# Performance work log

Measured on AMD Instinct MI355X. Metric: run time of the kernel, lower is better.

The kernel has to match this reference:

```python
import jax, jax.numpy as jnp
import numpy as np

N = 10000        # nodes
E = 160000       # active edges
NS = 128         # scalar (0e) channels per tensor
NV = 64          # vector (1o) channels per tensor
LAT = 64         # latent dim
AVG_NEIGH = 16.0
SQ2 = float(np.sqrt(2.0))
SQ3 = float(np.sqrt(3.0))
EPS = 1e-5


def setup_inputs() -> dict:
    key = jax.random.key(0)
    ks = jax.random.split(key, 24)
    rn = lambda k, s: jax.random.normal(k, s, jnp.float32)
    d = {}
    d["latents"] = rn(ks[0], (E, LAT))
    d["node_features"] = rn(ks[1], (N, NS + 3 * NV))
    d["edge_features"] = rn(ks[2], (E, NS + 3 * NV))
    d["edge_sh"] = rn(ks[3], (E, 4))
    d["edge_index"] = jax.random.randint(ks[4], (2, E), 0, N)
    d["atom_type"] = jax.random.randint(ks[5], (N,), 0, 10)
    d["active_edges"] = jnp.arange(E)
    # separable layer norm affine params (node and edge)
    d["g_s_n"] = jnp.ones((NS,), jnp.float32); d["b_s_n"] = jnp.zeros((NS,), jnp.float32)
    d["g_v_n"] = jnp.ones((NV,), jnp.float32)
    d["g_s_e"] = jnp.ones((NS,), jnp.float32); d["b_s_e"] = jnp.zeros((NS,), jnp.float32)
    d["g_v_e"] = jnp.ones((NV,), jnp.float32)
    # FullyConnectedTensorProduct weights (path-normalized init).
    # tp input: 2*NS scalars, 2*NV vectors; sh: 1 scalar + 1 vector;
    # tp output: NS+NV scalars (scalars+gates), NV vectors.
    nSt, nVt, nSo = 2 * NS, 2 * NV, NS + NV
    d["W_ss0"] = rn(ks[6], (nSt, nSo)) / np.sqrt(nSt * 2)
    d["W_vv0"] = rn(ks[7], (nVt, nSo)) / np.sqrt(nVt * 2)
    d["W_sv1"] = rn(ks[8], (nSt, NV)) / np.sqrt(nSt * 3)
    d["W_vs1"] = rn(ks[9], (nVt, NV)) / np.sqrt(nVt * 3)
    d["W_vv1"] = rn(ks[10], (nVt, NV)) / np.sqrt(nVt * 3)
    # lin_post (per-l channel mixing)
    d["Wp_s"] = rn(ks[11], (NS, NS)) / np.sqrt(NS)
    d["Wp_v"] = rn(ks[12], (NV, NV)) / np.sqrt(NV)
    # env_embed_mlps: single linear latent -> weight_numel (NS+NV channels)
    d["W_env"] = rn(ks[13], (LAT, NS + NV)) / np.sqrt(LAT)
    # linear_res
    d["Wr_s"] = rn(ks[14], (NS, NS)) / np.sqrt(NS)
    d["Wr_v"] = rn(ks[15], (NV, NV)) / np.sqrt(NV)
    return d


def _sep_ln(x, g_s, b_s, g_v):
    # separable layer norm: standard LN on scalars, RMS-of-norms on vectors
    s = x[:, :NS]
    v = x[:, NS:].reshape(-1, NV, 3)
    mu = s.mean(-1, keepdims=True)
    var = ((s - mu) ** 2).mean(-1, keepdims=True)
    s = (s - mu) * jax.lax.rsqrt(var + EPS) * g_s + b_s
    vn = jnp.mean(jnp.sum(v * v, -1), -1, keepdims=True)  # (B,1)
    v = v * jax.lax.rsqrt(vn + EPS)[:, :, None] * g_v[None, :, None]
    return s, v


def _forward(latents, node_features, edge_features, edge_sh, edge_index,
             atom_type, active_edges,
             g_s_n, b_s_n, g_v_n, g_s_e, b_s_e, g_v_e,
             W_ss0, W_vv0, W_sv1, W_vs1, W_vv1,
             Wp_s, Wp_v, W_env, Wr_s, Wr_v):
    ec = edge_index[0][active_edges]                      # (E,) center nodes
    ns, nv = _sep_ln(node_features, g_s_n, b_s_n, g_v_n)
    es, ev = _sep_ln(edge_features, g_s_e, b_s_e, g_v_e)
    S = jnp.concatenate([ns[ec], es], axis=-1)            # (E, 2*NS)
    V = jnp.concatenate([nv[ec], ev], axis=1)             # (E, 2*NV, 3)
    sh0 = edge_sh[:, :1]                                  # (E,1)
    sh1 = edge_sh[:, 1:]                                  # (E,3)
    # fully-connected tensor product (tp_in x sh -> gate input)
    dotV = jnp.einsum('ecd,ed->ec', V, sh1) / SQ3         # 1x1->0
    out0 = (S * sh0) @ W_ss0 + dotV @ W_vv0               # (E, NS+NV) scalars
    out_v = (S @ W_sv1)[:, :, None] * sh1[:, None, :]     # 0x1->1
    out_v = out_v + jnp.einsum('ecd,cf->efd', V, W_vs1) * sh0[:, :, None]  # 1x0->1
    cross = jnp.cross(V, sh1[:, None, :]) / SQ2           # 1x1->1
    out_v = out_v + jnp.einsum('ecd,cf->efd', cross, W_vv1)  # (E, NV, 3)
    # gate
    s = jax.nn.silu(out0[:, :NS])
    gates = jax.nn.sigmoid(out0[:, NS:])
    v = out_v * gates[:, :, None]
    # lin_post
    s = s @ Wp_s
    v = jnp.einsum('ecd,cf->efd', v, Wp_v)
    # env weights from latents (elementwise linear per channel)
    w = latents[active_edges] @ W_env                     # (E, NS+NV)
    s = s * w[:, :NS]
    v = v * w[:, NS:][:, :, None]
    msg = jnp.concatenate([s, v.reshape(-1, 3 * NV)], axis=-1)  # (E, 320)
    agg = jax.ops.segment_sum(msg, ec, num_segments=N)
    agg = agg * jnp.float32(1.0 / np.sqrt(AVG_NEIGH))
    # residual linear on raw node features
    rs = node_features[:, :NS] @ Wr_s
    rv = jnp.einsum('ncd,cf->nfd', node_features[:, NS:].reshape(-1, NV, 3), Wr_v)
    res = jnp.concatenate([rs, rv.reshape(-1, 3 * NV)], axis=-1)
    return res + agg


def reference(latents, node_features, edge_features, edge_sh, edge_index,
              atom_type, active_edges,
              g_s_n, b_s_n, g_v_n, g_s_e, b_s_e, g_v_e,
              W_ss0, W_vv0, W_sv1, W_vs1, W_vv1,
              Wp_s, Wp_v, W_env, Wr_s, Wr_v):
    return _forward(latents, node_features, edge_features, edge_sh, edge_index,
                    atom_type, active_edges,
                    g_s_n, b_s_n, g_v_n, g_s_e, b_s_e, g_v_e,
                    W_ss0, W_vv0, W_sv1, W_vs1, W_vv1,
                    Wp_s, Wp_v, W_env, Wr_s, Wr_v)
```

## Files before the change

kernel.cpp:

```cpp
#include <hip/hip_runtime.h>

#define N_NODES 10000
#define N_EDGES 160000
#define NSC 128
#define ROW 320
#define EPS_LN 1e-5f
#define INV_SQ2 0.70710678118654752440f
#define INV_SQ3 0.57735026918962576451f

typedef unsigned short bfraw;
typedef __attribute__((ext_vector_type(8))) short short8;
typedef __attribute__((ext_vector_type(4))) float float4x;
typedef __attribute__((ext_vector_type(2))) float float2x;

__device__ __forceinline__ float bf2f(bfraw u) {
    union { unsigned int i; float f; } x; x.i = ((unsigned int)u) << 16; return x.f;
}
__device__ __forceinline__ bfraw f2bf(float f) {
    union { float f; unsigned int i; } x; x.f = f;
    unsigned int i = x.i;
    unsigned int lsb = (i >> 16) & 1u;
    i += 0x7fffu + lsb;
    return (bfraw)(i >> 16);
}
template<bool B> __device__ __forceinline__ float LD(const void* p, size_t i) {
    if (B) return bf2f(((const bfraw*)p)[i]);
    else   return ((const float*)p)[i];
}
template<bool B> __device__ __forceinline__ void ST(void* p, size_t i, float v) {
    if (B) ((bfraw*)p)[i] = f2bf(v);
    else   ((float*)p)[i] = v;
}
__device__ __forceinline__ float wred64(float v) {
#pragma unroll
    for (int o = 32; o > 0; o >>= 1) v += __shfl_xor(v, o, 64);
    return v;
}
__device__ __forceinline__ void wredx12(float a[12]) {
#pragma unroll
    for (int o = 32; o > 0; o >>= 1) {
        float t[12];
#pragma unroll
        for (int i = 0; i < 12; i++) t[i] = __shfl_xor(a[i], o, 64);
#pragma unroll
        for (int i = 0; i < 12; i++) a[i] += t[i];
    }
}
__device__ __forceinline__ float silu_f(float x) { return x / (1.0f + __expf(-x)); }
__device__ __forceinline__ float sigm_f(float x) { return 1.0f / (1.0f + __expf(-x)); }

#define MFMA16(a, b, c) __builtin_amdgcn_mfma_f32_16x16x32_bf16((a), (b), (c), 0, 0, 0)

__device__ __forceinline__ int SDI(int r, int c) { return r * 384 + (c ^ ((r & 7) << 3)); }
__device__ __forceinline__ int X64(int r, int c) { return r * 64  + (c ^ ((r & 7) << 3)); }
__device__ __forceinline__ int SPI(int r, int c) { return r * 128 + (c ^ ((r & 7) << 3)); }
__device__ __forceinline__ int WVI(int r, int c) { return r * 192 + (c ^ ((r & 7) << 2)); }

__device__ __forceinline__ int dtype_flag(const void* g_s_n) {
    return (((const unsigned int*)g_s_n)[0] == 0x3F803F80u) ? 1 : 0;
}

__device__ __forceinline__ void pack_body(int idx, int fl,
    const void* Wss0, const void* Wvv0, const void* Wsv1, const void* Wvs1,
    const void* Wvv1, const void* Wps,  const void* Wpv,  const void* Wenv,
    const void* Wrs,  const void* Wrv,  bfraw* __restrict__ dst)
{
    const void* src; int K, N, base;
    if      (idx <  49152) { src = Wss0; K = 256; N = 192; base = 0; }
    else if (idx <  73728) { src = Wvv0; K = 128; N = 192; base = 49152; }
    else if (idx <  90112) { src = Wsv1; K = 256; N =  64; base = 73728; }
    else if (idx <  98304) { src = Wvs1; K = 128; N =  64; base = 90112; }
    else if (idx < 106496) { src = Wvv1; K = 128; N =  64; base = 98304; }
    else if (idx < 122880) { src = Wps;  K = 128; N = 128; base = 106496; }
    else if (idx < 126976) { src = Wpv;  K =  64; N =  64; base = 122880; }
    else if (idx < 139264) { src = Wenv; K =  64; N = 192; base = 126976; }
    else if (idx < 155648) { src = Wrs;  K = 128; N = 128; base = 139264; }
    else                   { src = Wrv;  K =  64; N =  64; base = 155648; }
    int li = idx - base;
    int j = li & 7, l = (li >> 3) & 63, t = li >> 9;
    int NT = N >> 4;
    int nt = t % NT, kt = t / NT;
    int k = kt * 32 + ((l >> 4) << 3) + j;
    int n = (nt << 4) + (l & 15);
    float v = fl ? bf2f(((const bfraw*)src)[(size_t)k * N + n])
                 : ((const float*)src)[(size_t)k * N + n];
    dst[idx] = f2bf(v);
}

template<bool B>
__device__ __forceinline__ void node_ln_body(int n, int lane,
    const void* nf, const void* g_s, const void* b_s, const void* g_v,
    float* __restrict__ nsnv)
{
    size_t base = (size_t)n * ROW;
    float s0 = LD<B>(nf, base + lane), s1 = LD<B>(nf, base + 64 + lane);
    float mu = wred64(s0 + s1) * (1.0f / 128.0f);
    float d0 = s0 - mu, d1 = s1 - mu;
    float var = wred64(d0 * d0 + d1 * d1) * (1.0f / 128.0f);
    float rs = rsqrtf(var + EPS_LN);
    float o0 = d0 * rs * LD<B>(g_s, lane) + LD<B>(b_s, lane);
    float o1 = d1 * rs * LD<B>(g_s, 64 + lane) + LD<B>(b_s, 64 + lane);
    float vx = LD<B>(nf, base + NSC + 3 * lane);
    float vy = LD<B>(nf, base + NSC + 3 * lane + 1);
    float vz = LD<B>(nf, base + NSC + 3 * lane + 2);
    float vn = wred64(vx * vx + vy * vy + vz * vz) * (1.0f / 64.0f);
    float rv = rsqrtf(vn + EPS_LN) * LD<B>(g_v, lane);
    float* o = nsnv + base;
    o[lane] = o0; o[64 + lane] = o1;
    o[NSC + 3 * lane] = vx * rv; o[NSC + 3 * lane + 1] = vy * rv; o[NSC + 3 * lane + 2] = vz * rv;
}

__global__ __launch_bounds__(256) void prep_k(
    const void* Wss0, const void* Wvv0, const void* Wsv1, const void* Wvs1,
    const void* Wvv1, const void* Wps,  const void* Wpv,  const void* Wenv,
    const void* Wrs,  const void* Wrv,  bfraw* __restrict__ pk,
    const int* __restrict__ eidx, const int* __restrict__ act, int* __restrict__ counts,
    const void* nf, const void* g_s_n, const void* b_s_n, const void* g_v_n,
    float* __restrict__ nsnv)
{
    int fl = dtype_flag(g_s_n);
    int idx = blockIdx.x * 256 + threadIdx.x;
    if (idx < 159744)
        pack_body(idx, fl, Wss0, Wvv0, Wsv1, Wvs1, Wvv1, Wps, Wpv, Wenv, Wrs, Wrv, pk);
    if (idx < N_EDGES)
        atomicAdd(&counts[eidx[act[idx]]], 1);
    int w = threadIdx.x >> 6, lane = threadIdx.x & 63;
    int n = blockIdx.x * 4 + w;
    if (fl) node_ln_body<true >(n, lane, nf, g_s_n, b_s_n, g_v_n, nsnv);
    else    node_ln_body<false>(n, lane, nf, g_s_n, b_s_n, g_v_n, nsnv);
}

__global__ __launch_bounds__(1024) void scan_k(const int* __restrict__ counts,
                                               int* __restrict__ starts) {
    __shared__ int wsum[16];
    int t = threadIdx.x;
    int lo = t * 10;
    int lanev = t & 63, wv = t >> 6;
    int c[10];
    int s = 0;
    if (lo < N_NODES) {
#pragma unroll
        for (int j = 0; j < 10; j++) { c[j] = counts[lo + j]; s += c[j]; }
    }
    int ps = s;
#pragma unroll
    for (int o = 1; o < 64; o <<= 1) {
        int u = __shfl_up(ps, o, 64);
        if (lanev >= o) ps += u;
    }
    if (lanev == 63) wsum[wv] = ps;
    __syncthreads();
    if (t == 0) {
        int acc = 0;
#pragma unroll
        for (int i = 0; i < 16; i++) { int v = wsum[i]; wsum[i] = acc; acc += v; }
        starts[N_NODES] = acc;
    }
    __syncthreads();
    if (lo < N_NODES) {
        int acc = wsum[wv] + ps - s;
#pragma unroll
        for (int j = 0; j < 10; j++) { starts[lo + j] = acc; acc += c[j]; }
    }
}

__global__ void fill_k(const int* __restrict__ eidx, const int* __restrict__ act,
                       const int* __restrict__ starts, int* __restrict__ cursor,
                       int* __restrict__ csr) {
    int e = blockIdx.x * 256 + threadIdx.x;
    if (e < N_EDGES) {
        int n = eidx[act[e]];
        int pos = atomicAdd(&cursor[n], 1);
        csr[starts[n] + pos] = e;
    }
}

template<bool B>
__device__ void edge_body(char* smem, int tid,
    const float* __restrict__ nsnv,
    const void* ef, const void* esh,
    const int* __restrict__ eidx, const int* __restrict__ act,
    const void* lat,
    const void* g_s_e, const void* b_s_e, const void* g_v_e,
    const bfraw* __restrict__ pk,
    bfraw* __restrict__ msg)
{
    bfraw* SD     = (bfraw*)(smem);
    bfraw* Vn     = (bfraw*)(smem + 12288);
    bfraw* Ve     = (bfraw*)(smem + 18432);
    bfraw* gate_u = (bfraw*)(smem + 18432);
    bfraw* sp_u   = (bfraw*)(smem + 20480);
    bfraw* lat_u  = (bfraw*)(smem + 24576);
    float* sh_f   = (float*)(smem + 26624);
    float* wenv_f = (float*)(smem);

    const bfraw* pWss0 = pk;
    const bfraw* pWvv0 = pk + 49152;
    const bfraw* pWsv1 = pk + 73728;
    const bfraw* pWvs1 = pk + 90112;
    const bfraw* pWvv1 = pk + 98304;
    const bfraw* pWps  = pk + 106496;
    const bfraw* pWpv  = pk + 122880;
    const bfraw* pWenv = pk + 126976;

    const int w = tid >> 6, lane = tid & 63;
    const int nl = lane & 15, mq = lane >> 4;
    const int e0 = blockIdx.x * 16;

    float gse0 = LD<B>(g_s_e, lane), gse1 = LD<B>(g_s_e, 64 + lane);
    float bse0 = LD<B>(b_s_e, lane), bse1 = LD<B>(b_s_e, 64 + lane);
    float gve  = LD<B>(g_v_e, lane);

    int ae_[4], cn_[4];
#pragma unroll
    for (int i = 0; i < 4; i++) ae_[i] = act[e0 + w * 4 + i];
#pragma unroll
    for (int i = 0; i < 4; i++) cn_[i] = eidx[ae_[i]];

    float es0[4], es1[4], ex[4], ey[4], ez[4];
    float shv[4][4];
#pragma unroll
    for (int i = 0; i < 4; i++) {
        int el = w * 4 + i, e = e0 + el;
        shv[i][0] = LD<B>(esh, (size_t)e * 4 + 0);
        shv[i][1] = LD<B>(esh, (size_t)e * 4 + 1);
        shv[i][2] = LD<B>(esh, (size_t)e * 4 + 2);
        shv[i][3] = LD<B>(esh, (size_t)e * 4 + 3);
        size_t eb = (size_t)e * ROW;
        es0[i] = LD<B>(ef, eb + lane);
        es1[i] = LD<B>(ef, eb + 64 + lane);
        ex[i]  = LD<B>(ef, eb + NSC + 3 * lane);
        ey[i]  = LD<B>(ef, eb + NSC + 3 * lane + 1);
        ez[i]  = LD<B>(ef, eb + NSC + 3 * lane + 2);
        float la = LD<B>(lat, (size_t)ae_[i] * 64 + lane);
        const float* nr = nsnv + (size_t)cn_[i] * ROW;
        float n0 = nr[lane], n1 = nr[64 + lane];
        float nx = nr[NSC + 3 * lane], ny = nr[NSC + 3 * lane + 1], nz = nr[NSC + 3 * lane + 2];
        SD[SDI(el, lane)]       = f2bf(n0);
        SD[SDI(el, 64 + lane)]  = f2bf(n1);
        SD[SDI(el, 256 + lane)] = f2bf((nx * shv[i][1] + ny * shv[i][2] + nz * shv[i][3]) * INV_SQ3);
        Vn[X64(el, lane)]       = f2bf(nx);
        Vn[X64(16 + el, lane)]  = f2bf(ny);
        Vn[X64(32 + el, lane)]  = f2bf(nz);
        lat_u[X64(el, lane)]    = f2bf(la);
        if (lane == 0) {
            sh_f[el * 4]     = shv[i][0]; sh_f[el * 4 + 1] = shv[i][1];
            sh_f[el * 4 + 2] = shv[i][2]; sh_f[el * 4 + 3] = shv[i][3];
        }
    }
    float red[12];
#pragma unroll
    for (int i = 0; i < 4; i++) {
        red[i]     = es0[i] + es1[i];
        red[4 + i] = es0[i] * es0[i] + es1[i] * es1[i];
        red[8 + i] = ex[i] * ex[i] + ey[i] * ey[i] + ez[i] * ez[i];
    }
    wredx12(red);
#pragma unroll
    for (int i = 0; i < 4; i++) {
        int el = w * 4 + i;
        float mu  = red[i] * (1.0f / 128.0f);
        float var = red[4 + i] * (1.0f / 128.0f) - mu * mu;
        float rs  = rsqrtf(var + EPS_LN);
        float o0  = (es0[i] - mu) * rs * gse0 + bse0;
        float o1  = (es1[i] - mu) * rs * gse1 + bse1;
        float rv  = rsqrtf(red[8 + i] * (1.0f / 64.0f) + EPS_LN) * gve;
        float exn = ex[i] * rv, eyn = ey[i] * rv, ezn = ez[i] * rv;
        SD[SDI(el, 128 + lane)] = f2bf(o0);
        SD[SDI(el, 192 + lane)] = f2bf(o1);
        SD[SDI(el, 320 + lane)] = f2bf((exn * shv[i][1] + eyn * shv[i][2] + ezn * shv[i][3]) * INV_SQ3);
        Ve[X64(el, lane)]       = f2bf(exn);
        Ve[X64(16 + el, lane)]  = f2bf(eyn);
        Ve[X64(32 + el, lane)]  = f2bf(ezn);
    }
    __syncthreads();

    float4x sA0={0,0,0,0}, sA1={0,0,0,0}, sA2={0,0,0,0}, cSV={0,0,0,0};
    {
        const bfraw* ps = pWss0 + (size_t)(3 * w * 64 + lane) * 8;
        const bfraw* pv = pWsv1 + (size_t)(w * 64 + lane) * 8;
        short8 b0[4], b1[4];
#define LDG1(kt, D) do { \
        D[0] = *(const short8*)(ps + (kt) * 6144);        \
        D[1] = *(const short8*)(ps + (kt) * 6144 + 512);  \
        D[2] = *(const short8*)(ps + (kt) * 6144 + 1024); \
        D[3] = *(const short8*)(pv + (kt) * 2048); } while (0)
        LDG1(0, b0); LDG1(1, b1);
#pragma unroll
        for (int kt = 0; kt < 8; kt++) {
            short8 a = *(const short8*)&SD[SDI(nl, kt * 32 + mq * 8)];
            if ((kt & 1) == 0) {
                sA0 = MFMA16(a, b0[0], sA0); sA1 = MFMA16(a, b0[1], sA1);
                sA2 = MFMA16(a, b0[2], sA2); cSV = MFMA16(a, b0[3], cSV);
                if (kt + 2 < 8) LDG1(kt + 2, b0);
            } else {
                sA0 = MFMA16(a, b1[0], sA0); sA1 = MFMA16(a, b1[1], sA1);
                sA2 = MFMA16(a, b1[2], sA2); cSV = MFMA16(a, b1[3], cSV);
                if (kt + 2 < 8) LDG1(kt + 2, b1);
            }
        }
#undef LDG1
    }
    float4x dA0={0,0,0,0}, dA1={0,0,0,0}, dA2={0,0,0,0};
    {
        const bfraw* pd = pWvv0 + (size_t)(3 * w * 64 + lane) * 8;
        short8 c0[3], c1[3];
#define LDGD(kt, D) do { \
        D[0] = *(const short8*)(pd + (kt) * 6144);        \
        D[1] = *(const short8*)(pd + (kt) * 6144 + 512);  \
        D[2] = *(const short8*)(pd + (kt) * 6144 + 1024); } while (0)
        LDGD(0, c0); LDGD(1, c1);
#pragma unroll
        for (int kt = 0; kt < 4; kt++) {
            short8 a = *(const short8*)&SD[SDI(nl, 256 + kt * 32 + mq * 8)];
            if ((kt & 1) == 0) {
                dA0 = MFMA16(a, c0[0], dA0); dA1 = MFMA16(a, c0[1], dA1); dA2 = MFMA16(a, c0[2], dA2);
                if (kt + 2 < 4) LDGD(kt + 2, c0);
            } else {
                dA0 = MFMA16(a, c1[0], dA0); dA1 = MFMA16(a, c1[1], dA1); dA2 = MFMA16(a, c1[2], dA2);
                if (kt + 2 < 4) LDGD(kt + 2, c1);
            }
        }
#undef LDGD
    }
    float o_g1[3][4];
#pragma unroll
    for (int r = 0; r < 4; r++) {
        float sh0 = sh_f[(mq * 4 + r) * 4];
        o_g1[0][r] = sh0 * sA0[r] + dA0[r];
        o_g1[1][r] = sh0 * sA1[r] + dA1[r];
        o_g1[2][r] = sh0 * sA2[r] + dA2[r];
    }
    float4x H[3] = {{0,0,0,0},{0,0,0,0},{0,0,0,0}};
    float4x K[3] = {{0,0,0,0},{0,0,0,0},{0,0,0,0}};
    {
        const bfraw* ph = pWvs1 + (size_t)(w * 64 + lane) * 8;
        const bfraw* pq = pWvv1 + (size_t)(w * 64 + lane) * 8;
        short8 gH0 = *(const short8*)(ph);
        short8 gH1 = *(const short8*)(ph + 2048);
        short8 gH2 = *(const short8*)(ph + 4096);
        short8 gH3 = *(const short8*)(ph + 6144);
        short8 gK0 = *(const short8*)(pq);
        short8 gK1 = *(const short8*)(pq + 2048);
        short8 gK2 = *(const short8*)(pq + 4096);
        short8 gK3 = *(const short8*)(pq + 6144);
#pragma unroll
        for (int d = 0; d < 3; d++) {
            short8 a0 = *(const short8*)&Vn[X64(d * 16 + nl, mq * 8)];
            short8 a1 = *(const short8*)&Vn[X64(d * 16 + nl, 32 + mq * 8)];
            short8 a2 = *(const short8*)&Ve[X64(d * 16 + nl, mq * 8)];
            short8 a3 = *(const short8*)&Ve[X64(d * 16 + nl, 32 + mq * 8)];
            H[d] = MFMA16(a0, gH0, H[d]); K[d] = MFMA16(a0, gK0, K[d]);
            H[d] = MFMA16(a1, gH1, H[d]); K[d] = MFMA16(a1, gK1, K[d]);
            H[d] = MFMA16(a2, gH2, H[d]); K[d] = MFMA16(a2, gK2, K[d]);
            H[d] = MFMA16(a3, gH3, H[d]); K[d] = MFMA16(a3, gK3, K[d]);
        }
    }
    __syncthreads();

#pragma unroll
    for (int t = 0; t < 3; t++) {
        int tile = 3 * w + t;
#pragma unroll
        for (int r = 0; r < 4; r++) {
            int el = mq * 4 + r;
            float o = o_g1[t][r];
            if (tile < 8) sp_u[SPI(el, tile * 16 + nl)]         = f2bf(silu_f(o));
            else          gate_u[X64(el, (tile - 8) * 16 + nl)] = f2bf(sigm_f(o));
        }
    }
    __syncthreads();

    {
        int f = w * 16 + nl;
#pragma unroll
        for (int r = 0; r < 4; r++) {
            int el = mq * 4 + r;
            float g   = bf2f(gate_u[X64(el, f)]);
            float svv = cSV[r];
            float s0v = sh_f[el * 4], b0 = sh_f[el * 4 + 1], b1 = sh_f[el * 4 + 2], b2 = sh_f[el * 4 + 3];
            float ov0 = svv * b0 + s0v * H[0][r] + (b2 * K[1][r] - b1 * K[2][r]) * INV_SQ2;
            float ov1 = svv * b1 + s0v * H[1][r] + (b0 * K[2][r] - b2 * K[0][r]) * INV_SQ2;
            float ov2 = svv * b2 + s0v * H[2][r] + (b1 * K[0][r] - b0 * K[1][r]) * INV_SQ2;
            Vn[X64(el, f)]      = f2bf(ov0 * g);
            Vn[X64(16 + el, f)] = f2bf(ov1 * g);
            Vn[X64(32 + el, f)] = f2bf(ov2 * g);
        }
    }
    __syncthreads();

    float4x s2_0 = {0,0,0,0}, s2_1 = {0,0,0,0};
    {
        const bfraw* pp = pWps + (size_t)(w * 64 + lane) * 8;
        short8 u0[2], u1[2];
#define LDS2(kt, D) do { \
        D[0] = *(const short8*)(pp + (kt) * 4096);         \
        D[1] = *(const short8*)(pp + (kt) * 4096 + 2048); } while (0)
        LDS2(0, u0); LDS2(1, u1);
#pragma unroll
        for (int kt = 0; kt < 4; kt++) {
            short8 a = *(const short8*)&sp_u[SPI(nl, kt * 32 + mq * 8)];
            if ((kt & 1) == 0) {
                s2_0 = MFMA16(a, u0[0], s2_0); s2_1 = MFMA16(a, u0[1], s2_1);
                if (kt + 2 < 4) LDS2(kt + 2, u0);
            } else {
                s2_0 = MFMA16(a, u1[0], s2_0); s2_1 = MFMA16(a, u1[1], s2_1);
                if (kt + 2 < 4) LDS2(kt + 2, u1);
            }
        }
#undef LDS2
    }
    float4x wv0 = {0,0,0,0}, wv1 = {0,0,0,0}, wv2 = {0,0,0,0};
    {
        const bfraw* pe = pWenv + (size_t)(3 * w * 64 + lane) * 8;
        short8 e00 = *(const short8*)(pe);
        short8 e01 = *(const short8*)(pe + 512);
        short8 e02 = *(const short8*)(pe + 1024);
        short8 e10 = *(const short8*)(pe + 6144);
        short8 e11 = *(const short8*)(pe + 6144 + 512);
        short8 e12 = *(const short8*)(pe + 6144 + 1024);
        short8 a0 = *(const short8*)&lat_u[X64(nl, mq * 8)];
        short8 a1 = *(const short8*)&lat_u[X64(nl, 32 + mq * 8)];
        wv0 = MFMA16(a0, e00, wv0); wv0 = MFMA16(a1, e10, wv0);
        wv1 = MFMA16(a0, e01, wv1); wv1 = MFMA16(a1, e11, wv1);
        wv2 = MFMA16(a0, e02, wv2); wv2 = MFMA16(a1, e12, wv2);
    }
    float4x v2[3] = {{0,0,0,0},{0,0,0,0},{0,0,0,0}};
    {
        const bfraw* pz = pWpv + (size_t)(w * 64 + lane) * 8;
        short8 z0 = *(const short8*)(pz);
        short8 z1 = *(const short8*)(pz + 2048);
#pragma unroll
        for (int d = 0; d < 3; d++) {
            short8 a0 = *(const short8*)&Vn[X64(d * 16 + nl, mq * 8)];
            short8 a1 = *(const short8*)&Vn[X64(d * 16 + nl, 32 + mq * 8)];
            v2[d] = MFMA16(a0, z0, v2[d]);
            v2[d] = MFMA16(a1, z1, v2[d]);
        }
    }
    {
        float4x wvv[3] = {wv0, wv1, wv2};
#pragma unroll
        for (int t = 0; t < 3; t++)
#pragma unroll
            for (int r = 0; r < 4; r++)
                wenv_f[WVI(mq * 4 + r, (3 * w + t) * 16 + nl)] = wvv[t][r];
    }
    __syncthreads();

#pragma unroll
    for (int t = 0; t < 2; t++) {
        int c = (w + 4 * t) * 16 + nl;
        float4x s2v = (t == 0) ? s2_0 : s2_1;
#pragma unroll
        for (int r = 0; r < 4; r++) {
            int el = mq * 4 + r;
            msg[(size_t)(e0 + el) * 320 + c] = f2bf(s2v[r] * wenv_f[WVI(el, c)]);
        }
    }
    {
        int f = w * 16 + nl;
#pragma unroll
        for (int r = 0; r < 4; r++) {
            int el = mq * 4 + r;
            float we = wenv_f[WVI(el, 128 + f)];
            size_t base = (size_t)(e0 + el) * 320 + NSC + 3 * f;
            msg[base]     = f2bf(v2[0][r] * we);
            msg[base + 1] = f2bf(v2[1][r] * we);
            msg[base + 2] = f2bf(v2[2][r] * we);
        }
    }
}

__global__ __launch_bounds__(256, 4) void edge_mfma_k(
    const float* __restrict__ nsnv,
    const void* ef, const void* esh,
    const int* __restrict__ eidx, const int* __restrict__ act,
    const void* lat,
    const void* g_s_e, const void* b_s_e, const void* g_v_e,
    const bfraw* __restrict__ pk,
    bfraw* __restrict__ msg, const void* g_s_n)
{
    __shared__ __align__(16) char smem[26880];
    if (dtype_flag(g_s_n))
        edge_body<true >(smem, threadIdx.x, nsnv, ef, esh, eidx, act, lat,
                         g_s_e, b_s_e, g_v_e, pk, msg);
    else
        edge_body<false>(smem, threadIdx.x, nsnv, ef, esh, eidx, act, lat,
                         g_s_e, b_s_e, g_v_e, pk, msg);
}

__device__ __forceinline__ float lo16(unsigned u) { return bf2f((bfraw)(u & 0xffffu)); }
__device__ __forceinline__ float hi16(unsigned u) { return bf2f((bfraw)(u >> 16)); }

__global__ __launch_bounds__(256) void gather_k(
    const bfraw* __restrict__ msg, const int* __restrict__ starts,
    const int* __restrict__ csr, float* __restrict__ agg)
{
    int w = threadIdx.x >> 6, lane = threadIdx.x & 63;
    int n = blockIdx.x * 4 + w;
    if (n >= N_NODES) return;
    int s0 = starts[n], s1 = starts[n + 1];
    bool half = lane < 32;
    float l0 = 0, h0 = 0, l1 = 0, h1 = 0, l2 = 0, h2 = 0;
    int i = s0;
    for (; i + 1 < s1; i += 2) {
        const unsigned* r0 = (const unsigned*)(msg + (size_t)csr[i] * 320);
        const unsigned* r1 = (const unsigned*)(msg + (size_t)csr[i + 1] * 320);
        unsigned a00 = r0[lane], a01 = r0[64 + lane];
        unsigned a10 = r1[lane], a11 = r1[64 + lane];
        unsigned a02 = half ? r0[128 + lane] : 0u;
        unsigned a12 = half ? r1[128 + lane] : 0u;
        l0 += lo16(a00) + lo16(a10); h0 += hi16(a00) + hi16(a10);
        l1 += lo16(a01) + lo16(a11); h1 += hi16(a01) + hi16(a11);
        l2 += lo16(a02) + lo16(a12); h2 += hi16(a02) + hi16(a12);
    }
    if (i < s1) {
        const unsigned* r = (const unsigned*)(msg + (size_t)csr[i] * 320);
        unsigned a0 = r[lane], a1 = r[64 + lane];
        unsigned a2 = half ? r[128 + lane] : 0u;
        l0 += lo16(a0); h0 += hi16(a0);
        l1 += lo16(a1); h1 += hi16(a1);
        l2 += lo16(a2); h2 += hi16(a2);
    }
    float* o = agg + (size_t)n * ROW;
    float2x v0 = {l0, h0}, v1 = {l1, h1}, v2 = {l2, h2};
    ((float2x*)o)[lane] = v0;
    ((float2x*)(o + 128))[lane] = v1;
    if (half) ((float2x*)(o + 256))[lane] = v2;
}

template<bool B>
__device__ void final_body(char* smem, int tid,
    const void* nf, const float* __restrict__ agg,
    const bfraw* __restrict__ pk, void* out)
{
    bfraw* Sn_u = (bfraw*)(smem);
    bfraw* Vn_u = (bfraw*)(smem + 8704);
    const bfraw* pWrs = pk + 139264;
    const bfraw* pWrv = pk + 155648;

    const int w = tid >> 6, lane = tid & 63;
    const int nl = lane & 15, mq = lane >> 4;
    const int n0b = blockIdx.x * 32;

    for (int i = 0; i < 8; i++) {
        int el = w * 8 + i;
        int n = n0b + el;
        bool ok = n < N_NODES;
        size_t base = (size_t)n * ROW;
        float a0 = ok ? LD<B>(nf, base + lane) : 0.0f;
        float a1 = ok ? LD<B>(nf, base + 64 + lane) : 0.0f;
        float vx = ok ? LD<B>(nf, base + NSC + 3 * lane) : 0.0f;
        float vy = ok ? LD<B>(nf, base + NSC + 3 * lane + 1) : 0.0f;
        float vz = ok ? LD<B>(nf, base + NSC + 3 * lane + 2) : 0.0f;
        Sn_u[el * 136 + lane]      = f2bf(a0);
        Sn_u[el * 136 + 64 + lane] = f2bf(a1);
        Vn_u[(el) * 72 + lane]      = f2bf(vx);
        Vn_u[(32 + el) * 72 + lane] = f2bf(vy);
        Vn_u[(64 + el) * 72 + lane] = f2bf(vz);
    }
    __syncthreads();

    {
        const int mt = w & 1, ntb = (w >> 1) * 4;
        float4x c[4] = {{0,0,0,0},{0,0,0,0},{0,0,0,0},{0,0,0,0}};
#pragma unroll
        for (int kt = 0; kt < 4; kt++) {
            short8 a = *(const short8*)&Sn_u[(mt * 16 + nl) * 136 + kt * 32 + mq * 8];
#pragma unroll
            for (int t = 0; t < 4; t++) {
                short8 b = *(const short8*)&pWrs[((kt * 8 + ntb + t) * 64 + lane) * 8];
                c[t] = MFMA16(a, b, c[t]);
            }
        }
#pragma unroll
        for (int t = 0; t < 4; t++) {
            int cc = (ntb + t) * 16 + nl;
#pragma unroll
            for (int r = 0; r < 4; r++) {
                int n = n0b + mt * 16 + mq * 4 + r;
                if (n < N_NODES) {
                    size_t o = (size_t)n * ROW + cc;
                    ST<B>(out, o, c[t][r] + 0.25f * agg[o]);
                }
            }
        }
    }
    {
        float4x c[3][2] = {{{0,0,0,0},{0,0,0,0}},{{0,0,0,0},{0,0,0,0}},{{0,0,0,0},{0,0,0,0}}};
#pragma unroll
        for (int d = 0; d < 3; d++)
#pragma unroll
            for (int h = 0; h < 2; h++)
#pragma unroll
                for (int kt = 0; kt < 2; kt++) {
                    short8 a = *(const short8*)&Vn_u[(d * 32 + h * 16 + nl) * 72 + kt * 32 + mq * 8];
                    short8 b = *(const short8*)&pWrv[((kt * 4 + w) * 64 + lane) * 8];
                    c[d][h] = MFMA16(a, b, c[d][h]);
                }
        int f = w * 16 + nl;
#pragma unroll
        for (int h = 0; h < 2; h++)
#pragma unroll
            for (int r = 0; r < 4; r++) {
                int n = n0b + h * 16 + mq * 4 + r;
                if (n < N_NODES) {
                    size_t o = (size_t)n * ROW + NSC + 3 * f;
                    ST<B>(out, o,     c[0][h][r] + 0.25f * agg[o]);
                    ST<B>(out, o + 1, c[1][h][r] + 0.25f * agg[o + 1]);
                    ST<B>(out, o + 2, c[2][h][r] + 0.25f * agg[o + 2]);
                }
            }
    }
}

__global__ __launch_bounds__(256) void final_mfma_k(
    const void* nf, const float* __restrict__ agg,
    const bfraw* __restrict__ pk, void* out, const void* g_s_n)
{
    __shared__ __align__(16) char smem[22528];
    if (dtype_flag(g_s_n)) final_body<true >(smem, threadIdx.x, nf, agg, pk, out);
    else                   final_body<false>(smem, threadIdx.x, nf, agg, pk, out);
}

extern "C" void kernel_launch(void* const* d_in, const int* in_sizes, int n_in,
                              void* d_out, int out_size, void* d_ws, size_t ws_size,
                              hipStream_t stream)
{
    const void* latents = d_in[0];
    const void* node_f  = d_in[1];
    const void* edge_f  = d_in[2];
    const void* edge_sh = d_in[3];
    const int* edge_index = (const int*)d_in[4];
    const int* active     = (const int*)d_in[6];
    const void* g_s_n = d_in[7];
    const void* b_s_n = d_in[8];
    const void* g_v_n = d_in[9];
    const void* g_s_e = d_in[10];
    const void* b_s_e = d_in[11];
    const void* g_v_e = d_in[12];

    char* ws = (char*)d_ws;
    float* agg    = (float*)(ws + 256);
    float* nsnv   = (float*)(ws + 12800256);
    bfraw* pk     = (bfraw*)(ws + 25600256);
    int*   counts = (int*)(ws + 25919744);
    int*   cursor = (int*)(ws + 25960704);
    int*   starts = (int*)(ws + 26001664);
    int*   csr    = (int*)(ws + 26042624);
    bfraw* msg    = (bfraw*)(ws + 26682624);

    hipMemsetAsync(counts, 0, 81920, stream);
    prep_k<<<2500, 256, 0, stream>>>(d_in[13], d_in[14], d_in[15], d_in[16],
        d_in[17], d_in[18], d_in[19], d_in[20], d_in[21], d_in[22], pk,
        edge_index, active, counts, node_f, g_s_n, b_s_n, g_v_n, nsnv);
    scan_k<<<1, 1024, 0, stream>>>(counts, starts);
    fill_k<<<625, 256, 0, stream>>>(edge_index, active, starts, cursor, csr);
    edge_mfma_k<<<N_EDGES / 16, 256, 0, stream>>>(nsnv, edge_f, edge_sh, edge_index, active,
        latents, g_s_e, b_s_e, g_v_e, pk, msg, g_s_n);
    gather_k<<<N_NODES / 4, 256, 0, stream>>>(msg, starts, csr, agg);
    final_mfma_k<<<(N_NODES + 31) / 32, 256, 0, stream>>>(node_f, agg, pk, (void*)d_out, g_s_n);
}
```

Measured before the change: 581.4 us.

## Write edge messages in CSR order, store node LN in bf16, vectorize loads

fill_k now records each edge's destination slot in CSR order, and the edge kernel writes its message row directly to that slot. gather_k can then stream contiguous message rows per node instead of indirecting through a CSR index array. The normalized node features are stored as bf16 with paired scalars and planar vector components, which halves that buffer and lets the edge kernel copy node values into shared memory without conversion. Loads of features, spherical harmonics and latents are widened to 2/4-element vectors, node LN variance is computed from the mean of squares, and edge-kernel launch bounds rise to 6 blocks per CU, at the cost of scattered message writes and some extra register pressure.

```diff
diff --git a/kernel.cpp b/kernel.cpp
--- a/kernel.cpp
+++ b/kernel.cpp
@@ -23,6 +23,11 @@
     i += 0x7fffu + lsb;
     return (bfraw)(i >> 16);
 }
+__device__ __forceinline__ unsigned cvt_pk_bf16(float lo, float hi) {
+    unsigned r;
+    asm("v_cvt_pk_bf16_f32 %0, %1, %2" : "=v"(r) : "v"(lo), "v"(hi));
+    return r;
+}
 template<bool B> __device__ __forceinline__ float LD(const void* p, size_t i) {
     if (B) return bf2f(((const bfraw*)p)[i]);
     else   return ((const float*)p)[i];
@@ -30,6 +35,29 @@
 template<bool B> __device__ __forceinline__ void ST(void* p, size_t i, float v) {
     if (B) ((bfraw*)p)[i] = f2bf(v);
     else   ((float*)p)[i] = v;
+}
+template<bool B> __device__ __forceinline__ float2x LD2(const void* p, size_t i) {
+    float2x r;
+    if (B) {
+        unsigned u = *(const unsigned*)((const bfraw*)p + i);
+        r.x = bf2f((bfraw)(u & 0xffffu)); r.y = bf2f((bfraw)(u >> 16));
+    } else {
+        r = *(const float2x*)((const float*)p + i);
+    }
+    return r;
+}
+template<bool B> __device__ __forceinline__ float4x LD4(const void* p, size_t i) {
+    float4x r;
+    if (B) {
+        unsigned long long u = *(const unsigned long long*)((const bfraw*)p + i);
+        r.x = bf2f((bfraw)(u & 0xffffu));
+        r.y = bf2f((bfraw)((u >> 16) & 0xffffu));
+        r.z = bf2f((bfraw)((u >> 32) & 0xffffu));
+        r.w = bf2f((bfraw)(u >> 48));
+    } else {
+        r = *(const float4x*)((const float*)p + i);
+    }
+    return r;
 }
 __device__ __forceinline__ float wred64(float v) {
 #pragma unroll
@@ -90,24 +118,26 @@
 template<bool B>
 __device__ __forceinline__ void node_ln_body(int n, int lane,
     const void* nf, const void* g_s, const void* b_s, const void* g_v,
-    float* __restrict__ nsnv)
+    bfraw* __restrict__ nsnv)
 {
     size_t base = (size_t)n * ROW;
-    float s0 = LD<B>(nf, base + lane), s1 = LD<B>(nf, base + 64 + lane);
-    float mu = wred64(s0 + s1) * (1.0f / 128.0f);
-    float d0 = s0 - mu, d1 = s1 - mu;
-    float var = wred64(d0 * d0 + d1 * d1) * (1.0f / 128.0f);
-    float rs = rsqrtf(var + EPS_LN);
-    float o0 = d0 * rs * LD<B>(g_s, lane) + LD<B>(b_s, lane);
-    float o1 = d1 * rs * LD<B>(g_s, 64 + lane) + LD<B>(b_s, 64 + lane);
+    float2x s = LD2<B>(nf, base + 2 * lane);
+    float mu = wred64(s.x + s.y) * (1.0f / 128.0f);
+    float m2 = wred64(s.x * s.x + s.y * s.y) * (1.0f / 128.0f);
+    float rs = rsqrtf(m2 - mu * mu + EPS_LN);
+    float2x g = LD2<B>(g_s, 2 * lane), b = LD2<B>(b_s, 2 * lane);
+    float o0 = (s.x - mu) * rs * g.x + b.x;
+    float o1 = (s.y - mu) * rs * g.y + b.y;
     float vx = LD<B>(nf, base + NSC + 3 * lane);
     float vy = LD<B>(nf, base + NSC + 3 * lane + 1);
     float vz = LD<B>(nf, base + NSC + 3 * lane + 2);
     float vn = wred64(vx * vx + vy * vy + vz * vz) * (1.0f / 64.0f);
     float rv = rsqrtf(vn + EPS_LN) * LD<B>(g_v, lane);
-    float* o = nsnv + base;
-    o[lane] = o0; o[64 + lane] = o1;
-    o[NSC + 3 * lane] = vx * rv; o[NSC + 3 * lane + 1] = vy * rv; o[NSC + 3 * lane + 2] = vz * rv;
+    bfraw* row = nsnv + (size_t)n * 320;
+    ((unsigned*)row)[lane] = cvt_pk_bf16(o0, o1);
+    row[128 + lane] = f2bf(vx * rv);
+    row[192 + lane] = f2bf(vy * rv);
+    row[256 + lane] = f2bf(vz * rv);
 }
 
 __global__ __launch_bounds__(256) void prep_k(
@@ -116,7 +146,7 @@
     const void* Wrs,  const void* Wrv,  bfraw* __restrict__ pk,
     const int* __restrict__ eidx, const int* __restrict__ act, int* __restrict__ counts,
     const void* nf, const void* g_s_n, const void* b_s_n, const void* g_v_n,
-    float* __restrict__ nsnv)
+    bfraw* __restrict__ nsnv)
 {
     int fl = dtype_flag(g_s_n);
     int idx = blockIdx.x * 256 + threadIdx.x;
@@ -166,20 +196,21 @@
 
 __global__ void fill_k(const int* __restrict__ eidx, const int* __restrict__ act,
                        const int* __restrict__ starts, int* __restrict__ cursor,
-                       int* __restrict__ csr) {
+                       int* __restrict__ inv) {
     int e = blockIdx.x * 256 + threadIdx.x;
     if (e < N_EDGES) {
         int n = eidx[act[e]];
         int pos = atomicAdd(&cursor[n], 1);
-        csr[starts[n] + pos] = e;
+        inv[e] = starts[n] + pos;
     }
 }
 
 template<bool B>
 __device__ void edge_body(char* smem, int tid,
-    const float* __restrict__ nsnv,
+    const bfraw* __restrict__ nsnv,
     const void* ef, const void* esh,
     const int* __restrict__ eidx, const int* __restrict__ act,
+    const int* __restrict__ inv,
     const void* lat,
     const void* g_s_e, const void* b_s_e, const void* g_v_e,
     const bfraw* __restrict__ pk,
@@ -192,6 +223,7 @@
     bfraw* sp_u   = (bfraw*)(smem + 20480);
     bfraw* lat_u  = (bfraw*)(smem + 24576);
     float* sh_f   = (float*)(smem + 26624);
+    int*   slot_s = (int*)(smem + 26880);
     float* wenv_f = (float*)(smem);
 
     const bfraw* pWss0 = pk;
@@ -207,13 +239,12 @@
     const int nl = lane & 15, mq = lane >> 4;
     const int e0 = blockIdx.x * 16;
 
-    float gse0 = LD<B>(g_s_e, lane), gse1 = LD<B>(g_s_e, 64 + lane);
-    float bse0 = LD<B>(b_s_e, lane), bse1 = LD<B>(b_s_e, 64 + lane);
+    float2x gse = LD2<B>(g_s_e, 2 * lane), bse = LD2<B>(b_s_e, 2 * lane);
     float gve  = LD<B>(g_v_e, lane);
 
-    int ae_[4], cn_[4];
-#pragma unroll
-    for (int i = 0; i < 4; i++) ae_[i] = act[e0 + w * 4 + i];
+    int ae_[4], cn_[4], sl_[4];
+#pragma unroll
+    for (int i = 0; i < 4; i++) { ae_[i] = act[e0 + w * 4 + i]; sl_[i] = inv[e0 + w * 4 + i]; }
 #pragma unroll
     for (int i = 0; i < 4; i++) cn_[i] = eidx[ae_[i]];
 
@@ -222,30 +253,31 @@
 #pragma unroll
     for (int i = 0; i < 4; i++) {
         int el = w * 4 + i, e = e0 + el;
-        shv[i][0] = LD<B>(esh, (size_t)e * 4 + 0);
-        shv[i][1] = LD<B>(esh, (size_t)e * 4 + 1);
-        shv[i][2] = LD<B>(esh, (size_t)e * 4 + 2);
-        shv[i][3] = LD<B>(esh, (size_t)e * 4 + 3);
+        float4x sh = LD4<B>(esh, (size_t)e * 4);
+        shv[i][0] = sh.x; shv[i][1] = sh.y; shv[i][2] = sh.z; shv[i][3] = sh.w;
         size_t eb = (size_t)e * ROW;
-        es0[i] = LD<B>(ef, eb + lane);
-        es1[i] = LD<B>(ef, eb + 64 + lane);
+        float2x es = LD2<B>(ef, eb + 2 * lane);
+        es0[i] = es.x; es1[i] = es.y;
         ex[i]  = LD<B>(ef, eb + NSC + 3 * lane);
         ey[i]  = LD<B>(ef, eb + NSC + 3 * lane + 1);
         ez[i]  = LD<B>(ef, eb + NSC + 3 * lane + 2);
-        float la = LD<B>(lat, (size_t)ae_[i] * 64 + lane);
-        const float* nr = nsnv + (size_t)cn_[i] * ROW;
-        float n0 = nr[lane], n1 = nr[64 + lane];
-        float nx = nr[NSC + 3 * lane], ny = nr[NSC + 3 * lane + 1], nz = nr[NSC + 3 * lane + 2];
-        SD[SDI(el, lane)]       = f2bf(n0);
-        SD[SDI(el, 64 + lane)]  = f2bf(n1);
-        SD[SDI(el, 256 + lane)] = f2bf((nx * shv[i][1] + ny * shv[i][2] + nz * shv[i][3]) * INV_SQ3);
-        Vn[X64(el, lane)]       = f2bf(nx);
-        Vn[X64(16 + el, lane)]  = f2bf(ny);
-        Vn[X64(32 + el, lane)]  = f2bf(nz);
-        lat_u[X64(el, lane)]    = f2bf(la);
+        const bfraw* nr = nsnv + (size_t)cn_[i] * 320;
+        unsigned nsp = ((const unsigned*)nr)[lane];
+        bfraw nvx = nr[128 + lane], nvy = nr[192 + lane], nvz = nr[256 + lane];
+        float nx = bf2f(nvx), ny = bf2f(nvy), nz = bf2f(nvz);
+        *(unsigned*)&SD[SDI(el, 2 * lane)] = nsp;
+        SD[SDI(el, 256 + lane)] = f2bf((nx * sh.y + ny * sh.z + nz * sh.w) * INV_SQ3);
+        Vn[X64(el, lane)]      = nvx;
+        Vn[X64(16 + el, lane)] = nvy;
+        Vn[X64(32 + el, lane)] = nvz;
+        if (lane < 32) {
+            float2x la = LD2<B>(lat, (size_t)ae_[i] * 64 + 2 * lane);
+            *(unsigned*)&lat_u[X64(el, 2 * lane)] = cvt_pk_bf16(la.x, la.y);
+        }
         if (lane == 0) {
-            sh_f[el * 4]     = shv[i][0]; sh_f[el * 4 + 1] = shv[i][1];
-            sh_f[el * 4 + 2] = shv[i][2]; sh_f[el * 4 + 3] = shv[i][3];
+            sh_f[el * 4]     = sh.x; sh_f[el * 4 + 1] = sh.y;
+            sh_f[el * 4 + 2] = sh.z; sh_f[el * 4 + 3] = sh.w;
+            slot_s[el] = sl_[i];
         }
     }
     float red[12];
@@ -262,12 +294,11 @@
         float mu  = red[i] * (1.0f / 128.0f);
         float var = red[4 + i] * (1.0f / 128.0f) - mu * mu;
         float rs  = rsqrtf(var + EPS_LN);
-        float o0  = (es0[i] - mu) * rs * gse0 + bse0;
-        float o1  = (es1[i] - mu) * rs * gse1 + bse1;
+        float o0  = (es0[i] - mu) * rs * gse.x + bse.x;
+        float o1  = (es1[i] - mu) * rs * gse.y + bse.y;
         float rv  = rsqrtf(red[8 + i] * (1.0f / 64.0f) + EPS_LN) * gve;
         float exn = ex[i] * rv, eyn = ey[i] * rv, ezn = ez[i] * rv;
-        SD[SDI(el, 128 + lane)] = f2bf(o0);
-        SD[SDI(el, 192 + lane)] = f2bf(o1);
+        *(unsigned*)&SD[SDI(el, 128 + 2 * lane)] = cvt_pk_bf16(o0, o1);
         SD[SDI(el, 320 + lane)] = f2bf((exn * shv[i][1] + eyn * shv[i][2] + ezn * shv[i][3]) * INV_SQ3);
         Ve[X64(el, lane)]       = f2bf(exn);
         Ve[X64(16 + el, lane)]  = f2bf(eyn);
@@ -448,6 +479,9 @@
     }
     __syncthreads();
 
+    int mslot[4];
+#pragma unroll
+    for (int r = 0; r < 4; r++) mslot[r] = slot_s[mq * 4 + r];
 #pragma unroll
     for (int t = 0; t < 2; t++) {
         int c = (w + 4 * t) * 16 + nl;
@@ -455,7 +489,7 @@
 #pragma unroll
         for (int r = 0; r < 4; r++) {
             int el = mq * 4 + r;
-            msg[(size_t)(e0 + el) * 320 + c] = f2bf(s2v[r] * wenv_f[WVI(el, c)]);
+            msg[(size_t)mslot[r] * 320 + c] = f2bf(s2v[r] * wenv_f[WVI(el, c)]);
         }
     }
     {
@@ -464,7 +498,7 @@
         for (int r = 0; r < 4; r++) {
             int el = mq * 4 + r;
             float we = wenv_f[WVI(el, 128 + f)];
-            size_t base = (size_t)(e0 + el) * 320 + NSC + 3 * f;
+            size_t base = (size_t)mslot[r] * 320 + NSC + 3 * f;
             msg[base]     = f2bf(v2[0][r] * we);
             msg[base + 1] = f2bf(v2[1][r] * we);
             msg[base + 2] = f2bf(v2[2][r] * we);
@@ -472,21 +506,22 @@
     }
 }
 
-__global__ __launch_bounds__(256, 4) void edge_mfma_k(
-    const float* __restrict__ nsnv,
+__global__ __launch_bounds__(256, 6) void edge_mfma_k(
+    const bfraw* __restrict__ nsnv,
     const void* ef, const void* esh,
     const int* __restrict__ eidx, const int* __restrict__ act,
+    const int* __restrict__ inv,
     const void* lat,
     const void* g_s_e, const void* b_s_e, const void* g_v_e,
     const bfraw* __restrict__ pk,
     bfraw* __restrict__ msg, const void* g_s_n)
 {
-    __shared__ __align__(16) char smem[26880];
+    __shared__ __align__(16) char smem[26944];
     if (dtype_flag(g_s_n))
-        edge_body<true >(smem, threadIdx.x, nsnv, ef, esh, eidx, act, lat,
+        edge_body<true >(smem, threadIdx.x, nsnv, ef, esh, eidx, act, inv, lat,
                          g_s_e, b_s_e, g_v_e, pk, msg);
     else
-        edge_body<false>(smem, threadIdx.x, nsnv, ef, esh, eidx, act, lat,
+        edge_body<false>(smem, threadIdx.x, nsnv, ef, esh, eidx, act, inv, lat,
                          g_s_e, b_s_e, g_v_e, pk, msg);
 }
 
@@ -495,7 +530,7 @@
 
 __global__ __launch_bounds__(256) void gather_k(
     const bfraw* __restrict__ msg, const int* __restrict__ starts,
-    const int* __restrict__ csr, float* __restrict__ agg)
+    float* __restrict__ agg)
 {
     int w = threadIdx.x >> 6, lane = threadIdx.x & 63;
     int n = blockIdx.x * 4 + w;
@@ -503,25 +538,36 @@
     int s0 = starts[n], s1 = starts[n + 1];
     bool half = lane < 32;
     float l0 = 0, h0 = 0, l1 = 0, h1 = 0, l2 = 0, h2 = 0;
-    int i = s0;
-    for (; i + 1 < s1; i += 2) {
-        const unsigned* r0 = (const unsigned*)(msg + (size_t)csr[i] * 320);
-        const unsigned* r1 = (const unsigned*)(msg + (size_t)csr[i + 1] * 320);
-        unsigned a00 = r0[lane], a01 = r0[64 + lane];
-        unsigned a10 = r1[lane], a11 = r1[64 + lane];
-        unsigned a02 = half ? r0[128 + lane] : 0u;
-        unsigned a12 = half ? r1[128 + lane] : 0u;
-        l0 += lo16(a00) + lo16(a10); h0 += hi16(a00) + hi16(a10);
-        l1 += lo16(a01) + lo16(a11); h1 += hi16(a01) + hi16(a11);
-        l2 += lo16(a02) + lo16(a12); h2 += hi16(a02) + hi16(a12);
-    }
-    if (i < s1) {
-        const unsigned* r = (const unsigned*)(msg + (size_t)csr[i] * 320);
-        unsigned a0 = r[lane], a1 = r[64 + lane];
-        unsigned a2 = half ? r[128 + lane] : 0u;
-        l0 += lo16(a0); h0 += hi16(a0);
-        l1 += lo16(a1); h1 += hi16(a1);
-        l2 += lo16(a2); h2 += hi16(a2);
+    const unsigned* p = (const unsigned*)msg + (size_t)s0 * 160;
+    int cnt = s1 - s0;
+    int i = 0;
+    for (; i + 3 < cnt; i += 4) {
+        const unsigned* r0 = p + (size_t)i * 160;
+        const unsigned* r1 = r0 + 160;
+        const unsigned* r2 = r0 + 320;
+        const unsigned* r3 = r0 + 480;
+        unsigned a0 = r0[lane], b0 = r0[64 + lane];
+        unsigned a1 = r1[lane], b1 = r1[64 + lane];
+        unsigned a2 = r2[lane], b2 = r2[64 + lane];
+        unsigned a3 = r3[lane], b3 = r3[64 + lane];
+        unsigned c0 = half ? r0[128 + lane] : 0u;
+        unsigned c1 = half ? r1[128 + lane] : 0u;
+        unsigned c2 = half ? r2[128 + lane] : 0u;
+        unsigned c3 = half ? r3[128 + lane] : 0u;
+        l0 += (lo16(a0) + lo16(a1)) + (lo16(a2) + lo16(a3));
+        h0 += (hi16(a0) + hi16(a1)) + (hi16(a2) + hi16(a3));
+        l1 += (lo16(b0) + lo16(b1)) + (lo16(b2) + lo16(b3));
+        h1 += (hi16(b0) + hi16(b1)) + (hi16(b2) + hi16(b3));
+        l2 += (lo16(c0) + lo16(c1)) + (lo16(c2) + lo16(c3));
+        h2 += (hi16(c0) + hi16(c1)) + (hi16(c2) + hi16(c3));
+    }
+    for (; i < cnt; i++) {
+        const unsigned* r = p + (size_t)i * 160;
+        unsigned a = r[lane], b = r[64 + lane];
+        unsigned c = half ? r[128 + lane] : 0u;
+        l0 += lo16(a); h0 += hi16(a);
+        l1 += lo16(b); h1 += hi16(b);
+        l2 += lo16(c); h2 += hi16(c);
     }
     float* o = agg + (size_t)n * ROW;
     float2x v0 = {l0, h0}, v1 = {l1, h1}, v2 = {l2, h2};
@@ -643,12 +689,12 @@
 
     char* ws = (char*)d_ws;
     float* agg    = (float*)(ws + 256);
-    float* nsnv   = (float*)(ws + 12800256);
+    bfraw* nsnv   = (bfraw*)(ws + 12800256);
     bfraw* pk     = (bfraw*)(ws + 25600256);
     int*   counts = (int*)(ws + 25919744);
     int*   cursor = (int*)(ws + 25960704);
     int*   starts = (int*)(ws + 26001664);
-    int*   csr    = (int*)(ws + 26042624);
+    int*   inv    = (int*)(ws + 26042624);
     bfraw* msg    = (bfraw*)(ws + 26682624);
 
     hipMemsetAsync(counts, 0, 81920, stream);
@@ -656,9 +702,9 @@
         d_in[17], d_in[18], d_in[19], d_in[20], d_in[21], d_in[22], pk,
         edge_index, active, counts, node_f, g_s_n, b_s_n, g_v_n, nsnv);
     scan_k<<<1, 1024, 0, stream>>>(counts, starts);
-    fill_k<<<625, 256, 0, stream>>>(edge_index, active, starts, cursor, csr);
+    fill_k<<<625, 256, 0, stream>>>(edge_index, active, starts, cursor, inv);
     edge_mfma_k<<<N_EDGES / 16, 256, 0, stream>>>(nsnv, edge_f, edge_sh, edge_index, active,
-        latents, g_s_e, b_s_e, g_v_e, pk, msg, g_s_n);
-    gather_k<<<N_NODES / 4, 256, 0, stream>>>(msg, starts, csr, agg);
+        inv, latents, g_s_e, b_s_e, g_v_e, pk, msg, g_s_n);
+    gather_k<<<N_NODES / 4, 256, 0, stream>>>(msg, starts, agg);
     final_mfma_k<<<(N_NODES + 31) / 32, 256, 0, stream>>>(node_f, agg, pk, (void*)d_out, g_s_n);
 }
```

After: 602.2 us. 1.04x slower.
